# Kernel tuning notes

Hardware: AMD Instinct MI355X
Metric: run time of the kernel (lower is better)

## Reference

```python
import jax, jax.numpy as jnp
import numpy as np

EPS = 1e-05
EPS_SQRT = EPS ** 0.5


def setup_inputs() -> dict:
    key = jax.random.key(0)
    x = jax.random.normal(key, (4, 2048, 4096), dtype=jnp.float32)
    weight = jnp.ones((4096,), dtype=jnp.float32)
    bias = jnp.zeros((4096,), dtype=jnp.float32)
    return {"x": x, "weight": weight, "bias": bias}


def _sign_nz(v):
    # sign() with 0 mapped to +1 (matches torch code: x_sign[x_sign==0]=1)
    s = jnp.sign(v)
    return jnp.where(s == 0, 1.0, s)


def _layer_normal_norm(x, weight, bias):
    # standardize over last dim (biased variance, correction=0)
    mean = jnp.mean(x, axis=-1, keepdims=True)
    var = jnp.var(x, axis=-1, keepdims=True)
    xs = (x - mean) / jnp.sqrt(var + EPS)

    x_sign = _sign_nz(xs)
    x_abs = jnp.abs(xs)
    l1p = jnp.log1p(x_abs)

    # Newton estimate of lambda (order 2)
    s1 = jnp.mean(x_sign * l1p, axis=-1, keepdims=True)
    d = (1.0 + x_abs) * l1p - x_abs
    dvar = 2.0 * jnp.mean(xs * d, axis=-1, keepdims=True)
    g1 = 0.5 * dvar - s1

    dmean = jnp.mean(d, axis=-1, keepdims=True)
    d_sub_sq = jnp.square(d - dmean)
    p1 = (1.0 + x_abs) * jnp.square(l1p) - 2.0 * d
    d2 = x_sign * p1
    d2var = 2.0 * jnp.mean(xs * d2 + d_sub_sq, axis=-1, keepdims=True)
    g2 = -0.5 * jnp.square(dvar) + 0.5 * d2var

    lmbda = 1.0 - g1 / (g2 + EPS_SQRT)  # broadcasts to full [B,S,D]

    # power transform
    eta = 1.0 + x_sign * (lmbda - 1.0)
    eta_sign = jax.lax.stop_gradient(_sign_nz(eta))
    exponent = eta + eta_sign * EPS_SQRT
    x_tr1 = (x_sign / exponent) * (jnp.power(1.0 + x_abs, exponent) - 1.0)
    x_tr2 = x_sign * l1p
    mask = jax.lax.stop_gradient(jnp.abs(eta) <= EPS_SQRT)
    x_tr = jnp.where(mask, x_tr2, x_tr1)

    # eval mode: no additive noise (self.training == False)
    return x_tr * weight + bias


def reference(x, weight, bias):
    return _layer_normal_norm(x, weight, bias)
```

## Files before the change

kernel.cpp:

```cpp
#include <hip/hip_runtime.h>
#include <math.h>

#define D 4096
#define NT 256
#define PER 16
#define EPS 1e-5f
#define EPS_SQRT 3.16227766016837933e-3f
#define LN2 0.69314718055994531f

__global__ __launch_bounds__(NT) void lnn_kernel(const float* __restrict__ x,
                                                 const float* __restrict__ w,
                                                 const float* __restrict__ b,
                                                 float* __restrict__ out) {
    const int row = blockIdx.x;
    const int tid = threadIdx.x;
    const float* xr = x + (size_t)row * D;
    float* orow = out + (size_t)row * D;

    __shared__ float red[4][8];

    float v[PER];
    const float4* x4 = (const float4*)xr;
#pragma unroll
    for (int c = 0; c < 4; ++c) {
        float4 f = x4[c * NT + tid];
        v[c*4+0] = f.x; v[c*4+1] = f.y; v[c*4+2] = f.z; v[c*4+3] = f.w;
    }

    float s = 0.f, s2 = 0.f;
#pragma unroll
    for (int i = 0; i < PER; ++i) { s += v[i]; s2 = fmaf(v[i], v[i], s2); }
#pragma unroll
    for (int o = 32; o > 0; o >>= 1) {
        s  += __shfl_down(s,  o, 64);
        s2 += __shfl_down(s2, o, 64);
    }
    const int wave = tid >> 6;
    if ((tid & 63) == 0) { red[wave][0] = s; red[wave][1] = s2; }
    __syncthreads();
    s  = red[0][0] + red[1][0] + red[2][0] + red[3][0];
    s2 = red[0][1] + red[1][1] + red[2][1] + red[3][1];
    const float inv_d = 1.f / (float)D;
    const float mean = s * inv_d;
    const float var  = s2 * inv_d - mean * mean;
    const float rstd = rsqrtf(var + EPS);

    float lp[PER];
    float s1 = 0.f, sxd = 0.f, sd = 0.f, sd2 = 0.f, sxd2 = 0.f;
#pragma unroll
    for (int i = 0; i < PER; ++i) {
        float xs = (v[i] - mean) * rstd;
        v[i] = xs;
        float ab = fabsf(xs);
        float L2 = __builtin_amdgcn_logf(1.f + ab);
        lp[i] = L2;
        float l  = L2 * LN2;
        float onea = 1.f + ab;
        float dd = fmaf(onea, l, -ab);
        s1   += copysignf(l, xs);
        sxd   = fmaf(xs, dd, sxd);
        sd   += dd;
        sd2   = fmaf(dd, dd, sd2);
        float ll = l * l;
        float p1 = fmaf(onea, ll, -(dd + dd));
        sxd2  = fmaf(ab, p1, sxd2);
    }
#pragma unroll
    for (int o = 32; o > 0; o >>= 1) {
        s1   += __shfl_down(s1,   o, 64);
        sxd  += __shfl_down(sxd,  o, 64);
        sd   += __shfl_down(sd,   o, 64);
        sd2  += __shfl_down(sd2,  o, 64);
        sxd2 += __shfl_down(sxd2, o, 64);
    }
    __syncthreads();
    if ((tid & 63) == 0) {
        red[wave][0] = s1; red[wave][1] = sxd; red[wave][2] = sd;
        red[wave][3] = sd2; red[wave][4] = sxd2;
    }
    __syncthreads();
    s1   = red[0][0] + red[1][0] + red[2][0] + red[3][0];
    sxd  = red[0][1] + red[1][1] + red[2][1] + red[3][1];
    sd   = red[0][2] + red[1][2] + red[2][2] + red[3][2];
    sd2  = red[0][3] + red[1][3] + red[2][3] + red[3][3];
    sxd2 = red[0][4] + red[1][4] + red[2][4] + red[3][4];

    const float dvar  = 2.f * sxd * inv_d;
    const float g1    = 0.5f * dvar - s1 * inv_d;
    const float dmean = sd * inv_d;
    const float vard  = sd2 * inv_d - dmean * dmean;
    const float d2var = 2.f * (sxd2 * inv_d + vard);
    const float g2    = -0.5f * dvar * dvar + 0.5f * d2var;
    const float lm    = 1.f - g1 * __builtin_amdgcn_rcpf(g2 + EPS_SQRT);

    const float eta_p = lm;
    const float eta_n = 2.f - lm;
    const float ep = eta_p + ((eta_p >= 0.f) ? EPS_SQRT : -EPS_SQRT);
    const float en = eta_n + ((eta_n >= 0.f) ? EPS_SQRT : -EPS_SQRT);
    const bool  mp = fabsf(eta_p) <= EPS_SQRT;
    const bool  mn = fabsf(eta_n) <= EPS_SQRT;
    const float rp =  __builtin_amdgcn_rcpf(ep);
    const float rn = -__builtin_amdgcn_rcpf(en);

    const float4* w4 = (const float4*)w;
    const float4* b4 = (const float4*)b;
#pragma unroll
    for (int c = 0; c < 4; ++c) {
        float4 wf = w4[c * NT + tid];
        float4 bf = b4[c * NT + tid];
        float wa[4] = {wf.x, wf.y, wf.z, wf.w};
        float ba[4] = {bf.x, bf.y, bf.z, bf.w};
        float oa[4];
#pragma unroll
        for (int j = 0; j < 4; ++j) {
            int i = c*4 + j;
            float xs = v[i];
            bool pos = (xs >= 0.f);
            float L2 = lp[i];
            float e  = pos ? ep : en;
            float re = pos ? rp : rn;
            bool  m  = pos ? mp : mn;
            float em = __builtin_amdgcn_exp2f(e * L2) - 1.f;
            float tr1 = re * em;
            float tr2 = copysignf(L2 * LN2, xs);
            float tr = m ? tr2 : tr1;
            oa[j] = fmaf(tr, wa[j], ba[j]);
        }
        float4 o = {oa[0], oa[1], oa[2], oa[3]};
        ((float4*)orow)[c * NT + tid] = o;
    }
}

extern "C" void kernel_launch(void* const* d_in, const int* in_sizes, int n_in,
                              void* d_out, int out_size, void* d_ws, size_t ws_size,
                              hipStream_t stream) {
    const float* x = (const float*)d_in[0];
    const float* w = (const float*)d_in[1];
    const float* b = (const float*)d_in[2];
    float* out = (float*)d_out;
    const int rows = in_sizes[0] / D;
    lnn_kernel<<<dim3(rows), dim3(NT), 0, stream>>>(x, w, b, out);
}
```

Before: 229.8 us.

## Process multiple rows per block with next-row prefetch and uniform fast path

Switches to a persistent-style grid of 2048 blocks, each looping over several rows and prefetching the next row's data into registers while the current row is computed. It stores the signed log instead of separate xs and log arrays, folds the normalization into an fma, and adds a warp-uniform branch that skips the mask select when neither eta is near zero. The aim is to hide global load latency and trim per-element ALU work, at the cost of more registers and fewer blocks in flight for a memory-bound kernel.

```diff
diff --git a/kernel.cpp b/kernel.cpp
--- a/kernel.cpp
+++ b/kernel.cpp
@@ -7,127 +7,179 @@
 #define EPS 1e-5f
 #define EPS_SQRT 3.16227766016837933e-3f
 #define LN2 0.69314718055994531f
+#define NBLOCKS 2048
 
 __global__ __launch_bounds__(NT) void lnn_kernel(const float* __restrict__ x,
                                                  const float* __restrict__ w,
                                                  const float* __restrict__ b,
-                                                 float* __restrict__ out) {
-    const int row = blockIdx.x;
+                                                 float* __restrict__ out,
+                                                 int rows, int rpb) {
     const int tid = threadIdx.x;
-    const float* xr = x + (size_t)row * D;
-    float* orow = out + (size_t)row * D;
+    const int wave = tid >> 6;
+    const int r0 = blockIdx.x * rpb;
+    int r1 = r0 + rpb; if (r1 > rows) r1 = rows;
+    if (r0 >= r1) return;
 
-    __shared__ float red[4][8];
+    __shared__ float red1[4][2];
+    __shared__ float red2[4][5];
+
+    const float inv_d = 1.f / (float)D;
 
     float v[PER];
-    const float4* x4 = (const float4*)xr;
+    {
+        const float4* x4 = (const float4*)(x + (size_t)r0 * D);
 #pragma unroll
-    for (int c = 0; c < 4; ++c) {
-        float4 f = x4[c * NT + tid];
-        v[c*4+0] = f.x; v[c*4+1] = f.y; v[c*4+2] = f.z; v[c*4+3] = f.w;
+        for (int c = 0; c < 4; ++c) {
+            float4 f = x4[c * NT + tid];
+            v[c*4+0] = f.x; v[c*4+1] = f.y; v[c*4+2] = f.z; v[c*4+3] = f.w;
+        }
     }
 
-    float s = 0.f, s2 = 0.f;
+    for (int r = r0; r < r1; ++r) {
+        const bool pn = (r + 1 < r1);
+        float n[PER];
+        if (pn) {
+            const float4* nx4 = (const float4*)(x + (size_t)(r + 1) * D);
 #pragma unroll
-    for (int i = 0; i < PER; ++i) { s += v[i]; s2 = fmaf(v[i], v[i], s2); }
+            for (int c = 0; c < 4; ++c) {
+                float4 f = nx4[c * NT + tid];
+                n[c*4+0] = f.x; n[c*4+1] = f.y; n[c*4+2] = f.z; n[c*4+3] = f.w;
+            }
+        }
+
+        float s = 0.f, s2 = 0.f;
 #pragma unroll
-    for (int o = 32; o > 0; o >>= 1) {
-        s  += __shfl_down(s,  o, 64);
-        s2 += __shfl_down(s2, o, 64);
-    }
-    const int wave = tid >> 6;
-    if ((tid & 63) == 0) { red[wave][0] = s; red[wave][1] = s2; }
-    __syncthreads();
-    s  = red[0][0] + red[1][0] + red[2][0] + red[3][0];
-    s2 = red[0][1] + red[1][1] + red[2][1] + red[3][1];
-    const float inv_d = 1.f / (float)D;
-    const float mean = s * inv_d;
-    const float var  = s2 * inv_d - mean * mean;
-    const float rstd = rsqrtf(var + EPS);
+        for (int i = 0; i < PER; ++i) { s += v[i]; s2 = fmaf(v[i], v[i], s2); }
+#pragma unroll
+        for (int o = 32; o > 0; o >>= 1) {
+            s  += __shfl_down(s,  o, 64);
+            s2 += __shfl_down(s2, o, 64);
+        }
+        if ((tid & 63) == 0) { red1[wave][0] = s; red1[wave][1] = s2; }
+        __syncthreads();
+        s  = red1[0][0] + red1[1][0] + red1[2][0] + red1[3][0];
+        s2 = red1[0][1] + red1[1][1] + red1[2][1] + red1[3][1];
+        const float mean = s * inv_d;
+        const float var  = s2 * inv_d - mean * mean;
+        const float rstd = rsqrtf(var + EPS);
+        const float nm   = -mean * rstd;
 
-    float lp[PER];
-    float s1 = 0.f, sxd = 0.f, sd = 0.f, sd2 = 0.f, sxd2 = 0.f;
+        float s1 = 0.f, sxd = 0.f, sd = 0.f, sd2 = 0.f, sxd2 = 0.f;
 #pragma unroll
-    for (int i = 0; i < PER; ++i) {
-        float xs = (v[i] - mean) * rstd;
-        v[i] = xs;
-        float ab = fabsf(xs);
-        float L2 = __builtin_amdgcn_logf(1.f + ab);
-        lp[i] = L2;
-        float l  = L2 * LN2;
-        float onea = 1.f + ab;
-        float dd = fmaf(onea, l, -ab);
-        s1   += copysignf(l, xs);
-        sxd   = fmaf(xs, dd, sxd);
-        sd   += dd;
-        sd2   = fmaf(dd, dd, sd2);
-        float ll = l * l;
-        float p1 = fmaf(onea, ll, -(dd + dd));
-        sxd2  = fmaf(ab, p1, sxd2);
-    }
+        for (int i = 0; i < PER; ++i) {
+            float xs   = fmaf(v[i], rstd, nm);
+            float ab   = fabsf(xs);
+            float onea = 1.f + ab;
+            float L2   = __builtin_amdgcn_logf(onea);
+            float sv   = copysignf(L2, xs);
+            v[i] = sv;
+            s1 += sv;
+            float l  = L2 * LN2;
+            float dd = fmaf(onea, l, -ab);
+            sxd = fmaf(xs, dd, sxd);
+            sd += dd;
+            sd2 = fmaf(dd, dd, sd2);
+            float p1 = fmaf(onea, l * l, -(dd + dd));
+            sxd2 = fmaf(ab, p1, sxd2);
+        }
+
+        float4 wfs[4], bfs[4];
+        {
+            const float4* w4 = (const float4*)w;
+            const float4* b4 = (const float4*)b;
 #pragma unroll
-    for (int o = 32; o > 0; o >>= 1) {
-        s1   += __shfl_down(s1,   o, 64);
-        sxd  += __shfl_down(sxd,  o, 64);
-        sd   += __shfl_down(sd,   o, 64);
-        sd2  += __shfl_down(sd2,  o, 64);
-        sxd2 += __shfl_down(sxd2, o, 64);
-    }
-    __syncthreads();
-    if ((tid & 63) == 0) {
-        red[wave][0] = s1; red[wave][1] = sxd; red[wave][2] = sd;
-        red[wave][3] = sd2; red[wave][4] = sxd2;
-    }
-    __syncthreads();
-    s1   = red[0][0] + red[1][0] + red[2][0] + red[3][0];
-    sxd  = red[0][1] + red[1][1] + red[2][1] + red[3][1];
-    sd   = red[0][2] + red[1][2] + red[2][2] + red[3][2];
-    sd2  = red[0][3] + red[1][3] + red[2][3] + red[3][3];
-    sxd2 = red[0][4] + red[1][4] + red[2][4] + red[3][4];
+            for (int c = 0; c < 4; ++c) {
+                wfs[c] = w4[c * NT + tid];
+                bfs[c] = b4[c * NT + tid];
+            }
+        }
 
-    const float dvar  = 2.f * sxd * inv_d;
-    const float g1    = 0.5f * dvar - s1 * inv_d;
-    const float dmean = sd * inv_d;
-    const float vard  = sd2 * inv_d - dmean * dmean;
-    const float d2var = 2.f * (sxd2 * inv_d + vard);
-    const float g2    = -0.5f * dvar * dvar + 0.5f * d2var;
-    const float lm    = 1.f - g1 * __builtin_amdgcn_rcpf(g2 + EPS_SQRT);
+#pragma unroll
+        for (int o = 32; o > 0; o >>= 1) {
+            s1   += __shfl_down(s1,   o, 64);
+            sxd  += __shfl_down(sxd,  o, 64);
+            sd   += __shfl_down(sd,   o, 64);
+            sd2  += __shfl_down(sd2,  o, 64);
+            sxd2 += __shfl_down(sxd2, o, 64);
+        }
+        if ((tid & 63) == 0) {
+            red2[wave][0] = s1; red2[wave][1] = sxd; red2[wave][2] = sd;
+            red2[wave][3] = sd2; red2[wave][4] = sxd2;
+        }
+        __syncthreads();
+        s1   = red2[0][0] + red2[1][0] + red2[2][0] + red2[3][0];
+        sxd  = red2[0][1] + red2[1][1] + red2[2][1] + red2[3][1];
+        sd   = red2[0][2] + red2[1][2] + red2[2][2] + red2[3][2];
+        sd2  = red2[0][3] + red2[1][3] + red2[2][3] + red2[3][3];
+        sxd2 = red2[0][4] + red2[1][4] + red2[2][4] + red2[3][4];
 
-    const float eta_p = lm;
-    const float eta_n = 2.f - lm;
-    const float ep = eta_p + ((eta_p >= 0.f) ? EPS_SQRT : -EPS_SQRT);
-    const float en = eta_n + ((eta_n >= 0.f) ? EPS_SQRT : -EPS_SQRT);
-    const bool  mp = fabsf(eta_p) <= EPS_SQRT;
-    const bool  mn = fabsf(eta_n) <= EPS_SQRT;
-    const float rp =  __builtin_amdgcn_rcpf(ep);
-    const float rn = -__builtin_amdgcn_rcpf(en);
+        const float s1m   = s1 * (inv_d * LN2);
+        const float dvar  = 2.f * sxd * inv_d;
+        const float g1    = 0.5f * dvar - s1m;
+        const float dmean = sd * inv_d;
+        const float vard  = sd2 * inv_d - dmean * dmean;
+        const float d2var = 2.f * (sxd2 * inv_d + vard);
+        const float g2    = -0.5f * dvar * dvar + 0.5f * d2var;
+        const float lm    = 1.f - g1 * __builtin_amdgcn_rcpf(g2 + EPS_SQRT);
 
-    const float4* w4 = (const float4*)w;
-    const float4* b4 = (const float4*)b;
+        const float eta_p = lm;
+        const float eta_n = 2.f - lm;
+        const float ep = eta_p + ((eta_p >= 0.f) ? EPS_SQRT : -EPS_SQRT);
+        const float en = eta_n + ((eta_n >= 0.f) ? EPS_SQRT : -EPS_SQRT);
+        const bool  mp = fabsf(eta_p) <= EPS_SQRT;
+        const bool  mn = fabsf(eta_n) <= EPS_SQRT;
+        const float rp =  __builtin_amdgcn_rcpf(ep);
+        const float rn = -__builtin_amdgcn_rcpf(en);
+
+        float* orow = out + (size_t)r * D;
+
+        if (!(mp || mn)) {
 #pragma unroll
-    for (int c = 0; c < 4; ++c) {
-        float4 wf = w4[c * NT + tid];
-        float4 bf = b4[c * NT + tid];
-        float wa[4] = {wf.x, wf.y, wf.z, wf.w};
-        float ba[4] = {bf.x, bf.y, bf.z, bf.w};
-        float oa[4];
+            for (int c = 0; c < 4; ++c) {
+                float wa[4] = {wfs[c].x, wfs[c].y, wfs[c].z, wfs[c].w};
+                float ba[4] = {bfs[c].x, bfs[c].y, bfs[c].z, bfs[c].w};
+                float oa[4];
 #pragma unroll
-        for (int j = 0; j < 4; ++j) {
-            int i = c*4 + j;
-            float xs = v[i];
-            bool pos = (xs >= 0.f);
-            float L2 = lp[i];
-            float e  = pos ? ep : en;
-            float re = pos ? rp : rn;
-            bool  m  = pos ? mp : mn;
-            float em = __builtin_amdgcn_exp2f(e * L2) - 1.f;
-            float tr1 = re * em;
-            float tr2 = copysignf(L2 * LN2, xs);
-            float tr = m ? tr2 : tr1;
-            oa[j] = fmaf(tr, wa[j], ba[j]);
+                for (int j = 0; j < 4; ++j) {
+                    float sv = v[c*4 + j];
+                    bool pos = (sv >= 0.f);
+                    float L2 = fabsf(sv);
+                    float e  = pos ? ep : en;
+                    float re = pos ? rp : rn;
+                    float tr = fmaf(re, __builtin_amdgcn_exp2f(e * L2), -re);
+                    oa[j] = fmaf(tr, wa[j], ba[j]);
+                }
+                float4 o = {oa[0], oa[1], oa[2], oa[3]};
+                ((float4*)orow)[c * NT + tid] = o;
+            }
+        } else {
+#pragma unroll
+            for (int c = 0; c < 4; ++c) {
+                float wa[4] = {wfs[c].x, wfs[c].y, wfs[c].z, wfs[c].w};
+                float ba[4] = {bfs[c].x, bfs[c].y, bfs[c].z, bfs[c].w};
+                float oa[4];
+#pragma unroll
+                for (int j = 0; j < 4; ++j) {
+                    float sv = v[c*4 + j];
+                    bool pos = (sv >= 0.f);
+                    float L2 = fabsf(sv);
+                    float e  = pos ? ep : en;
+                    float re = pos ? rp : rn;
+                    bool  m  = pos ? mp : mn;
+                    float tr1 = fmaf(re, __builtin_amdgcn_exp2f(e * L2), -re);
+                    float tr2 = sv * LN2;
+                    float tr  = m ? tr2 : tr1;
+                    oa[j] = fmaf(tr, wa[j], ba[j]);
+                }
+                float4 o = {oa[0], oa[1], oa[2], oa[3]};
+                ((float4*)orow)[c * NT + tid] = o;
+            }
         }
-        float4 o = {oa[0], oa[1], oa[2], oa[3]};
-        ((float4*)orow)[c * NT + tid] = o;
+
+        if (pn) {
+#pragma unroll
+            for (int i = 0; i < PER; ++i) v[i] = n[i];
+        }
     }
 }
 
@@ -139,5 +191,8 @@
     const float* b = (const float*)d_in[2];
     float* out = (float*)d_out;
     const int rows = in_sizes[0] / D;
-    lnn_kernel<<<dim3(rows), dim3(NT), 0, stream>>>(x, w, b, out);
+    int nblocks = NBLOCKS;
+    if (nblocks > rows) nblocks = rows;
+    const int rpb = (rows + nblocks - 1) / nblocks;
+    lnn_kernel<<<dim3(nblocks), dim3(NT), 0, stream>>>(x, w, b, out, rows, rpb);
 }
```

Result: slower. 238.8 us (+3.9%).
